# Kernel optimization log

Hardware: AMD Instinct MI355X
Metric: run time of the kernel (lower is better)

The kernel has to match this reference:

```python
import jax, jax.numpy as jnp
import numpy as np


def setup_inputs() -> dict:
    key = jax.random.key(0)
    k1, k2 = jax.random.split(key)
    inputs = jax.random.normal(k1, (2, 1600, 1600, 3), dtype=jnp.float32)
    # matches TruncatedNormal(stddev=20) scale of the learned offsets
    delta_p = 20.0 * jax.random.normal(k2, (2, 4, 4, 2), dtype=jnp.float32)
    return {"inputs": inputs, "delta_p": delta_p, "k": 4, "crop_size": 384}


def reference(inputs, delta_p, k, crop_size):
    # Faithful, gather-based version of the original dense bilinear-kernel sum:
    # G((x,y),(px,py)) = max(0,1-|x-px|)*max(0,1-|y-py|) summed over the whole
    # image == standard bilinear interpolation with zero padding outside.
    B, H, W, C = inputs.shape
    cs = crop_size
    pl = (H - cs * k) // 2
    pr = (W - cs * k) // 2
    s = jnp.arange(cs, dtype=jnp.float32)
    bi = jnp.arange(k, dtype=jnp.float32)
    # rows[t,i,j,s] = pl + i*cs + s + delta_p[t,i,j,0]
    rows = pl + bi[None, :, None, None] * cs + s[None, None, None, :] + delta_p[..., 0][..., None]
    # cols[t,i,j,s] = pr + j*cs + s + delta_p[t,i,j,1]
    cols = pr + bi[None, None, :, None] * cs + s[None, None, None, :] + delta_p[..., 1][..., None]
    rows = rows.reshape(B, -1)  # (B, k*k*cs), bin order i-major/j-minor as in the loop
    cols = cols.reshape(B, -1)

    def sample(img, r, c):
        # img (H,W,C); r,c (N,) fractional coords. 4-corner bilinear gather.
        r0 = jnp.floor(r)
        c0 = jnp.floor(c)
        rf = r - r0
        cf = c - c0
        out = jnp.zeros(r.shape + (img.shape[-1],), img.dtype)
        for dr, wr in ((0.0, 1.0 - rf), (1.0, rf)):
            ri = r0 + dr
            rvalid = (ri >= 0) & (ri < img.shape[0])
            rii = jnp.clip(ri, 0, img.shape[0] - 1).astype(jnp.int32)
            for dc, wc in ((0.0, 1.0 - cf), (1.0, cf)):
                ci = c0 + dc
                valid = rvalid & (ci >= 0) & (ci < img.shape[1])
                cii = jnp.clip(ci, 0, img.shape[1] - 1).astype(jnp.int32)
                w = jnp.where(valid, wr * wc, 0.0)
                out = out + w[:, None] * img[rii, cii]
        return out

    v = jax.vmap(sample)(inputs, rows, cols)  # (B, k*k*cs, C)
    # The original builds p with np.tile for BOTH axes, so every output row r
    # within a bin samples the same cs points -> rows are identical copies.
    v = v.reshape(B, k * k, 1, cs, C)
    return jnp.broadcast_to(v, (B, k * k, cs, cs, C))
```

## Files before the change

### kernel.cpp

```cpp
#include <hip/hip_runtime.h>


constexpr int B  = 2;
constexpr int H  = 1600;
constexpr int W  = 1600;
constexpr int C  = 3;
constexpr int K  = 4;
constexpr int CS = 384;
constexpr int PL = (H - CS * K) / 2;
constexpr int ROW_F  = CS * C;
constexpr int ROW_F4 = ROW_F / 4;
constexpr int RCHUNK = 8;
constexpr int NCHUNK = CS / RCHUNK;
constexpr int CHUNK_F4 = RCHUNK * ROW_F4;

__global__ __launch_bounds__(256) void roideform_kernel(
    const float* __restrict__ img,
    const float* __restrict__ dp,
    float* __restrict__ out)
{
    const int bid    = blockIdx.x;
    const int bbin   = bid / NCHUNK;
    const int rchunk = bid - bbin * NCHUNK;
    const int b      = bbin >> 4;
    const int bin    = bbin & 15;
    const int i      = bin >> 2;
    const int j      = bin & 3;

    __shared__ float vrow[ROW_F];

    const float dp0 = dp[((b * K + i) * K + j) * 2 + 0];
    const float dp1 = dp[((b * K + i) * K + j) * 2 + 1];
    const float* __restrict__ imgb = img + (size_t)b * H * W * C;

    for (int s = threadIdx.x; s < CS; s += blockDim.x) {
        const float r = (float)(PL + i * CS + s) + dp0;
        const float c = (float)(PL + j * CS + s) + dp1;
        const float r0 = floorf(r), c0 = floorf(c);
        const float rf = r - r0,   cf = c - c0;
        const int ri0 = (int)r0, ci0 = (int)c0;

        float acc0 = 0.f, acc1 = 0.f, acc2 = 0.f;
#pragma unroll
        for (int dr = 0; dr < 2; ++dr) {
            const int  ri = ri0 + dr;
            const float wr = dr ? rf : (1.0f - rf);
            const bool rvalid = (ri >= 0) && (ri < H);
#pragma unroll
            for (int dc = 0; dc < 2; ++dc) {
                const int  ci = ci0 + dc;
                const float wc = dc ? cf : (1.0f - cf);
                if (rvalid && (ci >= 0) && (ci < W)) {
                    const float w = wr * wc;
                    const float* p = imgb + ((size_t)ri * W + ci) * C;
                    acc0 += w * p[0];
                    acc1 += w * p[1];
                    acc2 += w * p[2];
                }
            }
        }
        vrow[s * 3 + 0] = acc0;
        vrow[s * 3 + 1] = acc1;
        vrow[s * 3 + 2] = acc2;
    }
    __syncthreads();

    const float4* __restrict__ v4 = (const float4*)vrow;
    float4* __restrict__ out4 =
        (float4*)out + (size_t)(bbin * CS + rchunk * RCHUNK) * ROW_F4;

    for (int t = threadIdx.x; t < CHUNK_F4; t += 256) {
        out4[t] = v4[t % ROW_F4];
    }
}

extern "C" void kernel_launch(void* const* d_in, const int* in_sizes, int n_in,
                              void* d_out, int out_size, void* d_ws, size_t ws_size,
                              hipStream_t stream) {
    const float* img = (const float*)d_in[0];
    const float* dp  = (const float*)d_in[1];
    float* out = (float*)d_out;

    const int grid = B * K * K * NCHUNK;
    roideform_kernel<<<grid, 256, 0, stream>>>(img, dp, out);
}
```

Measured before the change: 113.7 us.

## Split gather and broadcast into separate kernels to avoid redundant interpolation

Computes each bin's bilinearly interpolated row once in a gather kernel writing to workspace, then a second kernel loads that row into shared memory and replicates it across output rows with a fully unrolled store loop. This removes recomputation of the same gather in every row-chunk block. It adds an extra kernel launch and a small workspace write/read round trip.

```diff
diff --git a/kernel.cpp b/kernel.cpp
--- a/kernel.cpp
+++ b/kernel.cpp
@@ -10,67 +10,78 @@
 constexpr int PL = (H - CS * K) / 2;
 constexpr int ROW_F  = CS * C;
 constexpr int ROW_F4 = ROW_F / 4;
+constexpr int NBBIN  = B * K * K;
 constexpr int RCHUNK = 8;
 constexpr int NCHUNK = CS / RCHUNK;
-constexpr int CHUNK_F4 = RCHUNK * ROW_F4;
+constexpr int K2_ITERS = RCHUNK * ROW_F4 / 256;
 
-__global__ __launch_bounds__(256) void roideform_kernel(
+__global__ __launch_bounds__(128) void roideform_gather(
     const float* __restrict__ img,
     const float* __restrict__ dp,
-    float* __restrict__ out)
+    float* __restrict__ ws)
 {
-    const int bid    = blockIdx.x;
-    const int bbin   = bid / NCHUNK;
-    const int rchunk = bid - bbin * NCHUNK;
-    const int b      = bbin >> 4;
-    const int bin    = bbin & 15;
-    const int i      = bin >> 2;
-    const int j      = bin & 3;
-
-    __shared__ float vrow[ROW_F];
+    const int bbin = blockIdx.x / 3;
+    const int s    = (blockIdx.x % 3) * 128 + threadIdx.x;
+    const int b    = bbin >> 4;
+    const int bin  = bbin & 15;
+    const int i    = bin >> 2;
+    const int j    = bin & 3;
 
     const float dp0 = dp[((b * K + i) * K + j) * 2 + 0];
     const float dp1 = dp[((b * K + i) * K + j) * 2 + 1];
     const float* __restrict__ imgb = img + (size_t)b * H * W * C;
 
-    for (int s = threadIdx.x; s < CS; s += blockDim.x) {
-        const float r = (float)(PL + i * CS + s) + dp0;
-        const float c = (float)(PL + j * CS + s) + dp1;
-        const float r0 = floorf(r), c0 = floorf(c);
-        const float rf = r - r0,   cf = c - c0;
-        const int ri0 = (int)r0, ci0 = (int)c0;
+    const float r = (float)(PL + i * CS + s) + dp0;
+    const float c = (float)(PL + j * CS + s) + dp1;
+    const float r0 = floorf(r), c0 = floorf(c);
+    const float rf = r - r0,   cf = c - c0;
+    const int ri0 = (int)r0, ci0 = (int)c0;
 
-        float acc0 = 0.f, acc1 = 0.f, acc2 = 0.f;
+    float acc0 = 0.f, acc1 = 0.f, acc2 = 0.f;
 #pragma unroll
-        for (int dr = 0; dr < 2; ++dr) {
-            const int  ri = ri0 + dr;
-            const float wr = dr ? rf : (1.0f - rf);
-            const bool rvalid = (ri >= 0) && (ri < H);
+    for (int dr = 0; dr < 2; ++dr) {
+        const int  ri = ri0 + dr;
+        const float wr = dr ? rf : (1.0f - rf);
+        const bool rvalid = (ri >= 0) && (ri < H);
 #pragma unroll
-            for (int dc = 0; dc < 2; ++dc) {
-                const int  ci = ci0 + dc;
-                const float wc = dc ? cf : (1.0f - cf);
-                if (rvalid && (ci >= 0) && (ci < W)) {
-                    const float w = wr * wc;
-                    const float* p = imgb + ((size_t)ri * W + ci) * C;
-                    acc0 += w * p[0];
-                    acc1 += w * p[1];
-                    acc2 += w * p[2];
-                }
+        for (int dc = 0; dc < 2; ++dc) {
+            const int  ci = ci0 + dc;
+            const float wc = dc ? cf : (1.0f - cf);
+            if (rvalid && (ci >= 0) && (ci < W)) {
+                const float w = wr * wc;
+                const float* p = imgb + ((size_t)ri * W + ci) * C;
+                acc0 += w * p[0];
+                acc1 += w * p[1];
+                acc2 += w * p[2];
             }
         }
-        vrow[s * 3 + 0] = acc0;
-        vrow[s * 3 + 1] = acc1;
-        vrow[s * 3 + 2] = acc2;
     }
+    float* o = ws + ((size_t)bbin * CS + s) * C;
+    o[0] = acc0;
+    o[1] = acc1;
+    o[2] = acc2;
+}
+
+__global__ __launch_bounds__(256) void roideform_bcast(
+    const float* __restrict__ ws,
+    float* __restrict__ out)
+{
+    const int bid   = blockIdx.x;
+    const int bbin  = bid / NCHUNK;
+    const int chunk = bid - bbin * NCHUNK;
+
+    __shared__ float4 row[ROW_F4];
+    const float4* __restrict__ ws4 = (const float4*)ws + (size_t)bbin * ROW_F4;
+    for (int t = threadIdx.x; t < ROW_F4; t += 256) row[t] = ws4[t];
     __syncthreads();
 
-    const float4* __restrict__ v4 = (const float4*)vrow;
     float4* __restrict__ out4 =
-        (float4*)out + (size_t)(bbin * CS + rchunk * RCHUNK) * ROW_F4;
+        (float4*)out + (size_t)(bbin * CS + chunk * RCHUNK) * ROW_F4;
 
-    for (int t = threadIdx.x; t < CHUNK_F4; t += 256) {
-        out4[t] = v4[t % ROW_F4];
+#pragma unroll
+    for (int it = 0; it < K2_ITERS; ++it) {
+        const int t = it * 256 + (int)threadIdx.x;
+        out4[t] = row[t % ROW_F4];
     }
 }
 
@@ -80,7 +91,8 @@
     const float* img = (const float*)d_in[0];
     const float* dp  = (const float*)d_in[1];
     float* out = (float*)d_out;
+    float* ws  = (float*)d_ws;
 
-    const int grid = B * K * K * NCHUNK;
-    roideform_kernel<<<grid, 256, 0, stream>>>(img, dp, out);
+    roideform_gather<<<NBBIN * 3, 128, 0, stream>>>(img, dp, ws);
+    roideform_bcast<<<NBBIN * NCHUNK, 256, 0, stream>>>(ws, out);
 }
```

Result: faster. 106.5 us (-6.3%).
